# Performance work log

Hardware: AMD Instinct MI355X
Metric: run time of the kernel (lower is better)

Reference implementation:

```python
import jax, jax.numpy as jnp
import numpy as np

N = 100000      # nodes (accounts)
E = 500000      # edges (transactions)
F_NODE = 128
F_EDGE = 32
HEADS = 4
C = 64          # hidden_channels per head
HC = HEADS * C  # 256
OUT = 32
BN_EPS = 1e-5
NEG_SLOPE = 0.2


def setup_inputs() -> dict:
    key = jax.random.key(0)
    ks = jax.random.split(key, 24)
    rn = lambda k, shape, s=0.05: (jax.random.normal(k, shape, jnp.float32) * s)
    inp = {
        "x": jax.random.normal(ks[0], (N, F_NODE), jnp.float32),
        "edge_index": jax.random.randint(ks[1], (2, E), 0, N, dtype=jnp.int32),
        "edge_attr": jax.random.normal(ks[2], (E, F_EDGE), jnp.float32),
        # node_proj
        "Wp": rn(ks[3], (F_NODE, C)), "bp": jnp.zeros((C,), jnp.float32),
    }
    in_dims = [C, HC, HC]
    i = 4
    for l, d in enumerate(in_dims):
        inp[f"Wg{l}"] = rn(ks[i], (d, HC)); i += 1
        inp[f"as{l}"] = rn(ks[i], (HEADS, C)); i += 1
        inp[f"ad{l}"] = rn(ks[i], (HEADS, C)); i += 1
        inp[f"bg{l}"] = jnp.zeros((HC,), jnp.float32)
        inp[f"g{l}"] = jnp.ones((HC,), jnp.float32)   # BN gamma
        inp[f"be{l}"] = jnp.zeros((HC,), jnp.float32)  # BN beta
    inp["W1"] = rn(ks[i], (2 * HC + F_EDGE, OUT)); inp["b1"] = jnp.zeros((OUT,), jnp.float32)
    inp["W2"] = rn(ks[i + 1], (OUT, 1)); inp["b2"] = jnp.zeros((1,), jnp.float32)
    return inp


def _gat_layer(h, src, dst, Wg, att_s, att_d, bg):
    # PyG GATConv (concat=True, add_self_loops=False), eval mode (no dropout).
    xh = (h @ Wg).reshape(N, HEADS, C)                      # [N,H,C]
    a_s = jnp.sum(xh * att_s, axis=-1)                      # [N,H]
    a_d = jnp.sum(xh * att_d, axis=-1)                      # [N,H]
    e = jax.nn.leaky_relu(a_s[src] + a_d[dst], NEG_SLOPE)   # [E,H]
    m = jax.lax.stop_gradient(jax.ops.segment_max(e, dst, num_segments=N))
    ex = jnp.exp(e - m[dst])
    den = jax.ops.segment_sum(ex, dst, num_segments=N)      # [N,H]
    alpha = ex / (den[dst] + 1e-16)                         # softmax over in-edges of dst
    agg = jax.ops.segment_sum(xh[src] * alpha[:, :, None], dst, num_segments=N)
    return agg.reshape(N, HC) + bg


def _forward(x, edge_index, edge_attr, Wp, bp,
             Wg0, as0, ad0, bg0, g0, be0,
             Wg1, as1, ad1, bg1, g1, be1,
             Wg2, as2, ad2, bg2, g2, be2,
             W1, b1, W2, b2):
    src, dst = edge_index[0], edge_index[1]
    h = jax.nn.relu(x @ Wp + bp)                            # [N,64]
    bn_scale = 1.0 / jnp.sqrt(jnp.float32(1.0) + BN_EPS)    # BN eval: mean=0, var=1
    layers = [(Wg0, as0, ad0, bg0, g0, be0),
              (Wg1, as1, ad1, bg1, g1, be1),
              (Wg2, as2, ad2, bg2, g2, be2)]
    for Wg, a_s, a_d, bg, g, be in layers:
        hn = _gat_layer(h, src, dst, Wg, a_s, a_d, bg)
        hn = jax.nn.relu(hn * (g * bn_scale) + be)          # BatchNorm(eval) + ReLU
        h = h + hn if h.shape == hn.shape else hn           # residual (skipped at layer 0)
    # decode_edges: MLP(src_emb || dst_emb || edge_attr) without materializing the concat:
    W1s, W1d, W1e = W1[:HC], W1[HC:2 * HC], W1[2 * HC:]
    z = jax.nn.relu((h @ W1s)[src] + (h @ W1d)[dst] + edge_attr @ W1e + b1)  # [E,32]
    return (z @ W2 + b2)[:, 0]                              # [E] fraud logits


def reference(x, edge_index, edge_attr, Wp, bp,
              Wg0, as0, ad0, bg0, g0, be0,
              Wg1, as1, ad1, bg1, g1, be1,
              Wg2, as2, ad2, bg2, g2, be2,
              W1, b1, W2, b2):
    return _forward(x, edge_index, edge_attr, Wp, bp,
                    Wg0, as0, ad0, bg0, g0, be0,
                    Wg1, as1, ad1, bg1, g1, be1,
                    Wg2, as2, ad2, bg2, g2, be2,
                    W1, b1, W2, b2)
```

## Files before the change

kernel.cpp:

```cpp
#include <hip/hip_runtime.h>
#include <hip/hip_fp16.h>

#define NN 100000
#define EE 500000
#define F_NODE 128
#define F_EDGE 32
#define HEADS 4
#define CC 64
#define HC 256
#define OUTD 32
#define NEG_SLOPE 0.2f
#define BN_SCALE 0.9999950000374997f
#define NB_SCAN 391
#define MPAD 100096

using half8 = __attribute__((ext_vector_type(8))) _Float16;
using f32x4 = __attribute__((ext_vector_type(4))) float;

typedef const __attribute__((address_space(1))) void* gas_ptr;
typedef __attribute__((address_space(3))) void* las_ptr;

template<int K, int NOUT, int MODE, int ATT, int AF32>
__global__ __launch_bounds__(256, 2) void mgemm2(const __half* __restrict__ A,
                                                 const __half* __restrict__ Wt,
                                                 const float* __restrict__ bias,
                                                 __half* __restrict__ C,
                                                 const float* __restrict__ as_,
                                                 const float* __restrict__ ad_,
                                                 float* __restrict__ a_s,
                                                 float* __restrict__ a_d,
                                                 const float* __restrict__ A32) {
    constexpr int BM = 128;
    constexpr int BN = (NOUT >= 128) ? 128 : 64;
    constexpr int MI = 4;
    constexpr int NI = BN / 32;
    constexpr int KS = K / 64;
    constexpr int ABYTES = BM * 128;
    constexpr int BBYTES = BN * 128;
    __shared__ char smem[2 * (ABYTES + BBYTES)];

    const int tid  = threadIdx.x;
    const int wave = tid >> 6, lane = tid & 63;
    const int wr = wave >> 1, wc = wave & 1;
    const int lrow = lane & 15, kq = lane >> 4;
    const int m0 = blockIdx.x * BM;
    const int n0 = blockIdx.y * BN;
    const int srow = tid >> 3;
    const int sunit = tid & 7;
    const int wofs = (tid & 192) * 16;

    auto stageA16 = [&](int buf, int ks) {
        char* base = smem + buf * (ABYTES + BBYTES);
        const int kk = ks * 64;
#pragma unroll
        for (int it = 0; it < 4; ++it) {
            const int r = srow + it * 32;
            const __half* src = A + (size_t)(m0 + r) * K + kk + ((sunit ^ (r & 7)) << 3);
            __builtin_amdgcn_global_load_lds((gas_ptr)src,
                (las_ptr)(base + it * 4096 + wofs), 16, 0, 0);
        }
    };
    auto stageB = [&](int buf, int ks) {
        char* base = smem + buf * (ABYTES + BBYTES);
        const int kk = ks * 64;
#pragma unroll
        for (int it = 0; it < BN / 32; ++it) {
            const int r = srow + it * 32;
            const __half* src = Wt + (size_t)(n0 + r) * K + kk + ((sunit ^ (r & 7)) << 3);
            __builtin_amdgcn_global_load_lds((gas_ptr)src,
                (las_ptr)(base + ABYTES + it * 4096 + wofs), 16, 0, 0);
        }
    };

    float4 ar[4][2];
    auto loadA32 = [&](int ks) {
        const int kk = ks * 64;
#pragma unroll
        for (int it = 0; it < 4; ++it) {
            int rg = m0 + srow + it * 32;
            rg = (rg < NN) ? rg : NN - 1;
            const float* sp = A32 + (size_t)rg * K + kk + sunit * 8;
            ar[it][0] = *(const float4*)sp;
            ar[it][1] = *(const float4*)(sp + 4);
        }
    };
    auto writeA32 = [&](int buf) {
        char* base = smem + buf * (ABYTES + BBYTES);
#pragma unroll
        for (int it = 0; it < 4; ++it) {
            const int r = srow + it * 32;
            half8 hv;
            hv[0] = (_Float16)ar[it][0].x; hv[1] = (_Float16)ar[it][0].y;
            hv[2] = (_Float16)ar[it][0].z; hv[3] = (_Float16)ar[it][0].w;
            hv[4] = (_Float16)ar[it][1].x; hv[5] = (_Float16)ar[it][1].y;
            hv[6] = (_Float16)ar[it][1].z; hv[7] = (_Float16)ar[it][1].w;
            *(half8*)(base + r * 128 + ((sunit ^ (r & 7)) << 4)) = hv;
        }
    };

    f32x4 acc[MI][NI] = {};

    auto compute = [&](int buf) {
        const char* Ab = smem + buf * (ABYTES + BBYTES);
        const char* Bb = Ab + ABYTES;
#pragma unroll
        for (int k32 = 0; k32 < 2; ++k32) {
            const int ku = k32 * 4 + kq;
            half8 af[MI], bf[NI];
#pragma unroll
            for (int mi = 0; mi < MI; ++mi) {
                const int rr = wr * 64 + mi * 16 + lrow;
                af[mi] = *(const half8*)(Ab + rr * 128 + ((ku ^ (rr & 7)) << 4));
            }
#pragma unroll
            for (int ni = 0; ni < NI; ++ni) {
                const int rc = wc * (BN / 2) + ni * 16 + lrow;
                bf[ni] = *(const half8*)(Bb + rc * 128 + ((ku ^ (rc & 7)) << 4));
            }
#pragma unroll
            for (int mi = 0; mi < MI; ++mi)
#pragma unroll
                for (int ni = 0; ni < NI; ++ni)
                    acc[mi][ni] = __builtin_amdgcn_mfma_f32_16x16x32_f16(
                        af[mi], bf[ni], acc[mi][ni], 0, 0, 0);
        }
    };

    if constexpr (AF32) { loadA32(0); stageB(0, 0); writeA32(0); }
    else                { stageA16(0, 0); stageB(0, 0); }
    __syncthreads();
    int cur = 0;
#pragma unroll
    for (int ks = 0; ks < KS; ++ks) {
        if (ks + 1 < KS) {
            if constexpr (AF32) { loadA32(ks + 1); stageB(cur ^ 1, ks + 1); }
            else                { stageA16(cur ^ 1, ks + 1); stageB(cur ^ 1, ks + 1); }
        }
        compute(cur);
        if constexpr (AF32) { if (ks + 1 < KS) writeA32(cur ^ 1); }
        __syncthreads();
        cur ^= 1;
    }

    const int crow = kq * 4;
#pragma unroll
    for (int mi = 0; mi < MI; ++mi) {
#pragma unroll
        for (int ni = 0; ni < NI; ++ni) {
            const int col = n0 + wc * (BN / 2) + ni * 16 + lrow;
            float bcol = (MODE == 1) ? bias[col] : 0.f;
#pragma unroll
            for (int r = 0; r < 4; ++r) {
                float v = acc[mi][ni][r];
                if constexpr (MODE == 1) v = fmaxf(v + bcol, 0.f);
                const int row = m0 + wr * 64 + mi * 16 + crow + r;
                C[(size_t)row * NOUT + col] = __float2half(v);
            }
        }
    }

    if constexpr (ATT) {
        const int head = (n0 + wc * 64) >> 6;
        float wsv[NI], wdv[NI];
#pragma unroll
        for (int ni = 0; ni < NI; ++ni) {
            const int col = n0 + wc * (BN / 2) + ni * 16 + lrow;
            wsv[ni] = as_[col];
            wdv[ni] = ad_[col];
        }
#pragma unroll
        for (int mi = 0; mi < MI; ++mi) {
#pragma unroll
            for (int r = 0; r < 4; ++r) {
                float ss = 0.f, dd = 0.f;
#pragma unroll
                for (int ni = 0; ni < NI; ++ni) {
                    ss += acc[mi][ni][r] * wsv[ni];
                    dd += acc[mi][ni][r] * wdv[ni];
                }
#pragma unroll
                for (int off = 8; off >= 1; off >>= 1) {
                    ss += __shfl_xor(ss, off, 64);
                    dd += __shfl_xor(dd, off, 64);
                }
                if (lrow == 0) {
                    const int row = m0 + wr * 64 + mi * 16 + crow + r;
                    a_s[row * HEADS + head] = ss;
                    a_d[row * HEADS + head] = dd;
                }
            }
        }
    }
}

#define PREP_TOTAL (8192 + 16384 + 65536 + 65536 + 16384 + 1024)
__global__ __launch_bounds__(256) void prep_all(const float* __restrict__ Wp,
                                                const float* __restrict__ Wg0,
                                                const float* __restrict__ Wg1,
                                                const float* __restrict__ Wg2,
                                                const float* __restrict__ W1,
                                                __half* __restrict__ wpt,
                                                __half* __restrict__ wg0t,
                                                __half* __restrict__ wg1t,
                                                __half* __restrict__ wg2t,
                                                __half* __restrict__ w1t,
                                                __half* __restrict__ w1et) {
    int idx = blockIdx.x * 256 + threadIdx.x;
    if (idx < 8192) {
        int n = idx >> 7, k = idx & 127;
        wpt[idx] = __float2half(Wp[k * 64 + n]);
    } else if (idx < 24576) {
        int i = idx - 8192;
        int n = i >> 6, k = i & 63;
        wg0t[i] = __float2half(Wg0[k * 256 + n]);
    } else if (idx < 90112) {
        int i = idx - 24576;
        int n = i >> 8, k = i & 255;
        wg1t[i] = __float2half(Wg1[k * 256 + n]);
    } else if (idx < 155648) {
        int i = idx - 90112;
        int n = i >> 8, k = i & 255;
        wg2t[i] = __float2half(Wg2[k * 256 + n]);
    } else if (idx < 172032) {
        int i = idx - 155648;
        int n = i >> 8, k = i & 255;
        float v = (n < 32) ? W1[k * 32 + n] : W1[(256 + k) * 32 + (n - 32)];
        w1t[i] = __float2half(v);
    } else if (idx < PREP_TOTAL) {
        int i = idx - 172032;
        int n = i >> 5, k = i & 31;
        w1et[i] = __float2half(W1[2 * HC * OUTD + k * 32 + n]);
    }
}

__global__ __launch_bounds__(256) void csr_count(const int* __restrict__ dst,
                                                 int* __restrict__ deg,
                                                 int* __restrict__ pos) {
    int e = blockIdx.x * 256 + threadIdx.x;
    if (e >= EE) return;
    pos[e] = atomicAdd(deg + dst[e], 1);
}

__device__ __forceinline__ int wave_incl_scan(int v, int lane) {
#pragma unroll
    for (int off = 1; off < 64; off <<= 1) {
        int t = __shfl_up(v, off, 64);
        if (lane >= off) v += t;
    }
    return v;
}

__global__ __launch_bounds__(256) void scan1(const int* __restrict__ deg,
                                             int* __restrict__ rowptr,
                                             int* __restrict__ bsum) {
    int tid = threadIdx.x, n = blockIdx.x * 256 + tid;
    int lane = tid & 63, wave = tid >> 6;
    int d = (n < NN) ? deg[n] : 0;
    int v = wave_incl_scan(d, lane);
    __shared__ int ws[4];
    if (lane == 63) ws[wave] = v;
    __syncthreads();
    int woff = 0;
    for (int w = 0; w < wave; ++w) woff += ws[w];
    int incl = v + woff;
    if (n < NN) rowptr[n] = incl - d;
    if (tid == 255) bsum[blockIdx.x] = incl;
}

__global__ __launch_bounds__(512) void scan2(const int* __restrict__ bsum,
                                             int* __restrict__ boff) {
    int t = threadIdx.x;
    int lane = t & 63, wave = t >> 6;
    int d = (t < NB_SCAN) ? bsum[t] : 0;
    int v = wave_incl_scan(d, lane);
    __shared__ int ws[8];
    if (lane == 63) ws[wave] = v;
    __syncthreads();
    int woff = 0;
    for (int w = 0; w < wave; ++w) woff += ws[w];
    if (t < NB_SCAN) boff[t] = v + woff - d;
}

__global__ __launch_bounds__(256) void scan3(int* __restrict__ rowptr,
                                             const int* __restrict__ boff) {
    int n = blockIdx.x * 256 + threadIdx.x;
    if (n == 0) rowptr[NN] = EE;
    if (n < NN) rowptr[n] += boff[blockIdx.x];
}

__global__ __launch_bounds__(256) void csr_scatter(const int* __restrict__ src,
                                                   const int* __restrict__ dst,
                                                   const int* __restrict__ rowptr,
                                                   const int* __restrict__ pos,
                                                   int* __restrict__ srcs) {
    int e = blockIdx.x * 256 + threadIdx.x;
    if (e >= EE) return;
    srcs[rowptr[dst[e]] + pos[e]] = src[e];
}

__global__ __launch_bounds__(256) void gather_agg(const int* __restrict__ rowptr,
                                                  const int* __restrict__ srcs,
                                                  const float* __restrict__ a_s,
                                                  const float* __restrict__ a_d,
                                                  const __half* __restrict__ xh,
                                                  const float* __restrict__ bg,
                                                  const float* __restrict__ g,
                                                  const float* __restrict__ be,
                                                  __half* __restrict__ h,
                                                  int residual) {
    const int n = blockIdx.x * 4 + (threadIdx.x >> 6);
    const int lane = threadIdx.x & 63;
    const int hl = lane >> 5;
    const int l5 = lane & 31;
    const int hd = l5 >> 3;
    const int c0 = l5 * 8;

    const int start = rowptr[n], end = rowptr[n + 1];
    const float adv = a_d[n * HEADS + hd];

    float acc[8] = {};
    float den = 0.f;

    for (int i = start + hl; i < end; i += 8) {
        int  j1 = (i + 2 < end) ? i + 2 : i;
        int  j2 = (i + 4 < end) ? i + 4 : i;
        int  j3 = (i + 6 < end) ? i + 6 : i;
        const int s0 = srcs[i], s1 = srcs[j1], s2 = srcs[j2], s3 = srcs[j3];

        float v0 = a_s[s0 * HEADS + hd] + adv;
        float v1 = a_s[s1 * HEADS + hd] + adv;
        float v2 = a_s[s2 * HEADS + hd] + adv;
        float v3 = a_s[s3 * HEADS + hd] + adv;
        v0 = fmaxf(v0, v0 * NEG_SLOPE);
        v1 = fmaxf(v1, v1 * NEG_SLOPE);
        v2 = fmaxf(v2, v2 * NEG_SLOPE);
        v3 = fmaxf(v3, v3 * NEG_SLOPE);
        float e0 = __expf(v0);
        float e1 = (i + 2 < end) ? __expf(v1) : 0.f;
        float e2 = (i + 4 < end) ? __expf(v2) : 0.f;
        float e3 = (i + 6 < end) ? __expf(v3) : 0.f;

        half8 r0 = *(const half8*)(xh + (size_t)s0 * HC + c0);
        half8 r1 = *(const half8*)(xh + (size_t)s1 * HC + c0);
        half8 r2 = *(const half8*)(xh + (size_t)s2 * HC + c0);
        half8 r3 = *(const half8*)(xh + (size_t)s3 * HC + c0);

#pragma unroll
        for (int k = 0; k < 8; ++k)
            acc[k] += e0 * (float)r0[k] + e1 * (float)r1[k]
                    + e2 * (float)r2[k] + e3 * (float)r3[k];
        den += e0 + e1 + e2 + e3;
    }

    den += __shfl_xor(den, 32, 64);
#pragma unroll
    for (int k = 0; k < 8; ++k) acc[k] += __shfl_xor(acc[k], 32, 64);

    if (hl != 0) return;
    const float inv = 1.f / (den + 1e-16f);

    float bgv[8], gv[8], bev[8];
    *(float4*)(bgv)     = *(const float4*)(bg + c0);
    *(float4*)(bgv + 4) = *(const float4*)(bg + c0 + 4);
    *(float4*)(gv)      = *(const float4*)(g + c0);
    *(float4*)(gv + 4)  = *(const float4*)(g + c0 + 4);
    *(float4*)(bev)     = *(const float4*)(be + c0);
    *(float4*)(bev + 4) = *(const float4*)(be + c0 + 4);

    half8* hp = (half8*)(h + (size_t)n * HC + c0);
    float r[8];
#pragma unroll
    for (int k = 0; k < 8; ++k)
        r[k] = fmaxf((acc[k] * inv + bgv[k]) * (gv[k] * BN_SCALE) + bev[k], 0.f);
    if (residual) {
        half8 old = *hp;
#pragma unroll
        for (int k = 0; k < 8; ++k) r[k] += (float)old[k];
    }
    half8 o;
#pragma unroll
    for (int k = 0; k < 8; ++k) o[k] = (_Float16)r[k];
    __builtin_nontemporal_store(o, hp);
}

__global__ __launch_bounds__(256) void edge_final(const float* __restrict__ ea,
                                                  const __half* __restrict__ w1et,
                                                  const float* __restrict__ b1,
                                                  const int* __restrict__ src,
                                                  const int* __restrict__ dst,
                                                  const __half* __restrict__ hshd,
                                                  const float* __restrict__ W2,
                                                  const float* __restrict__ b2,
                                                  float* __restrict__ out) {
    __shared__ float zl[64][36];
    const int wave = threadIdx.x >> 6, lane = threadIdx.x & 63;
    const int e0 = blockIdx.x * 64;
    const int lrow = lane & 15, kofs = (lane >> 4) * 8;

    int er = e0 + wave * 16 + lrow;
    if (er >= EE) er = EE - 1;
    const float* ap = ea + (size_t)er * F_EDGE + kofs;
    float4 f0 = *(const float4*)ap;
    float4 f1 = *(const float4*)(ap + 4);
    half8 a;
    a[0] = (_Float16)f0.x; a[1] = (_Float16)f0.y;
    a[2] = (_Float16)f0.z; a[3] = (_Float16)f0.w;
    a[4] = (_Float16)f1.x; a[5] = (_Float16)f1.y;
    a[6] = (_Float16)f1.z; a[7] = (_Float16)f1.w;

    half8 b0 = *(const half8*)(w1et + (size_t)lrow * 32 + kofs);
    half8 b1v = *(const half8*)(w1et + (size_t)(16 + lrow) * 32 + kofs);
    f32x4 acc0 = {}, acc1 = {};
    acc0 = __builtin_amdgcn_mfma_f32_16x16x32_f16(a, b0,  acc0, 0, 0, 0);
    acc1 = __builtin_amdgcn_mfma_f32_16x16x32_f16(a, b1v, acc1, 0, 0, 0);

    const int crow = (lane >> 4) * 4;
    const float bc0 = b1[lrow], bc1 = b1[16 + lrow];
#pragma unroll
    for (int r = 0; r < 4; ++r) {
        zl[wave * 16 + crow + r][lrow]      = acc0[r] + bc0;
        zl[wave * 16 + crow + r][16 + lrow] = acc1[r] + bc1;
    }
    __syncthreads();

    const int el = threadIdx.x >> 2, j0 = (threadIdx.x & 3) * 8;
    const int e = e0 + el;
    const bool ok = e < EE;
    const int s = ok ? src[e] : 0;
    const int d = ok ? dst[e] : 0;

    half8 hs = *(const half8*)(hshd + (size_t)s * 64 + j0);
    half8 hdv = *(const half8*)(hshd + (size_t)d * 64 + 32 + j0);
    float w2v[8];
    *(float4*)(w2v)     = *(const float4*)(W2 + j0);
    *(float4*)(w2v + 4) = *(const float4*)(W2 + j0 + 4);
    float4 z0 = *(const float4*)&zl[el][j0];
    float4 z1 = *(const float4*)&zl[el][j0 + 4];

    float acc = 0.f;
    const float* zp0 = &z0.x;
    const float* zp1 = &z1.x;
#pragma unroll
    for (int i = 0; i < 4; ++i) {
        float z = zp0[i] + (float)hs[i] + (float)hdv[i];
        acc += fmaxf(z, 0.f) * w2v[i];
    }
#pragma unroll
    for (int i = 0; i < 4; ++i) {
        float z = zp1[i] + (float)hs[4 + i] + (float)hdv[4 + i];
        acc += fmaxf(z, 0.f) * w2v[4 + i];
    }
    acc += __shfl_xor(acc, 1, 64);
    acc += __shfl_xor(acc, 2, 64);
    if (ok && (threadIdx.x & 3) == 0) out[e] = acc + b2[0];
}

extern "C" void kernel_launch(void* const* d_in, const int* in_sizes, int n_in,
                              void* d_out, int out_size, void* d_ws, size_t ws_size,
                              hipStream_t stream) {
    const float* x  = (const float*)d_in[0];
    const int*   ei = (const int*)d_in[1];
    const float* ea = (const float*)d_in[2];
    const float* Wp = (const float*)d_in[3];
    const float* bp = (const float*)d_in[4];
    const float* W1 = (const float*)d_in[23];
    const float* b1 = (const float*)d_in[24];
    const float* W2 = (const float*)d_in[25];
    const float* b2 = (const float*)d_in[26];
    const int* src = ei;
    const int* dst = ei + EE;

    float* ws = (float*)d_ws;
    __half* h      = (__half*)(ws);
    __half* xh     = (__half*)(ws + 12820000);
    __half* h0     = (__half*)(ws + 32050000);
    __half* hshd   = (__half*)(ws + 35260000);
    float*  a_s    = ws + 38470000;
    float*  a_d    = ws + 38880000;
    int*    rowptr = (int*)(ws + 41270000);
    int*    deg    = (int*)(ws + 41380000);
    int*    pos    = (int*)(ws + 41480000);
    int*    srcs   = (int*)(ws + 42490000);
    int*    bsum   = (int*)(ws + 42990000);
    int*    boff   = (int*)(ws + 42991000);
    __half* wpt    = (__half*)(ws + 42992000);
    __half* wg0t   = (__half*)(ws + 43000000);
    __half* wg1t   = (__half*)(ws + 43010000);
    __half* wg2t   = (__half*)(ws + 43045000);
    __half* w1t    = (__half*)(ws + 43080000);
    __half* w1et   = (__half*)(ws + 43090000);
    float*  out    = (float*)d_out;

    const int MB = MPAD / 128;

    hipMemsetAsync(deg, 0, (size_t)NN * sizeof(int), stream);
    prep_all<<<(PREP_TOTAL + 255) / 256, 256, 0, stream>>>(
        Wp, (const float*)d_in[5], (const float*)d_in[11], (const float*)d_in[17],
        W1, wpt, wg0t, wg1t, wg2t, w1t, w1et);
    csr_count<<<(EE + 255) / 256, 256, 0, stream>>>(dst, deg, pos);
    scan1<<<NB_SCAN, 256, 0, stream>>>(deg, rowptr, bsum);
    scan2<<<1, 512, 0, stream>>>(bsum, boff);
    scan3<<<NB_SCAN, 256, 0, stream>>>(rowptr, boff);
    csr_scatter<<<(EE + 255) / 256, 256, 0, stream>>>(src, dst, rowptr, pos, srcs);

    mgemm2<F_NODE, 64, 1, 0, 1><<<dim3(MB, 1), 256, 0, stream>>>(
        nullptr, wpt, bp, h0, nullptr, nullptr, nullptr, nullptr, x);

    const __half* wgt_l[3] = {wg0t, wg1t, wg2t};
    for (int l = 0; l < 3; ++l) {
        const float* as_ = (const float*)d_in[6 + 6 * l];
        const float* ad_ = (const float*)d_in[7 + 6 * l];
        const float* bg  = (const float*)d_in[8 + 6 * l];
        const float* g   = (const float*)d_in[9 + 6 * l];
        const float* be  = (const float*)d_in[10 + 6 * l];

        if (l == 0) {
            mgemm2<CC, HC, 0, 1, 0><<<dim3(MB, 2), 256, 0, stream>>>(
                h0, wgt_l[0], nullptr, xh, as_, ad_, a_s, a_d, nullptr);
        } else {
            mgemm2<HC, HC, 0, 1, 0><<<dim3(MB, 2), 256, 0, stream>>>(
                h, wgt_l[l], nullptr, xh, as_, ad_, a_s, a_d, nullptr);
        }

        gather_agg<<<NN / 4, 256, 0, stream>>>(rowptr, srcs, a_s, a_d, xh,
                                               bg, g, be, h, l > 0 ? 1 : 0);
    }

    mgemm2<HC, 64, 0, 0, 0><<<dim3(MB, 1), 256, 0, stream>>>(
        h, w1t, nullptr, hshd, nullptr, nullptr, nullptr, nullptr, nullptr);

    edge_final<<<(EE + 63) / 64, 256, 0, stream>>>(ea, w1et, b1, src, dst,
                                                   hshd, W2, b2, out);
}
```

Measured before the change: 374.3 us.

## Reorder layer-0 GAT to aggregate 64-dim inputs before projecting with block-diagonal weights

Layer 0 now computes attention logits directly from the 64-dim projected features using precomputed Wg0·att vectors. It aggregates the 64-wide h0 rows per head instead of the 256-wide xh rows, then applies a block-diagonal 256x256 GEMM whose epilogue adds bias, BatchNorm and ReLU. The aim is to cut gather bandwidth in the first layer by a factor of four. The cost is two extra small kernels and a GEMM that is four times larger than before, three quarters of it multiplying zeros. Rounding changes slightly because the aggregated values are stored as fp16 before projection.

```diff
diff --git a/kernel.cpp b/kernel.cpp
--- a/kernel.cpp
+++ b/kernel.cpp
@@ -29,7 +29,10 @@
                                                  const float* __restrict__ ad_,
                                                  float* __restrict__ a_s,
                                                  float* __restrict__ a_d,
-                                                 const float* __restrict__ A32) {
+                                                 const float* __restrict__ A32,
+                                                 const float* __restrict__ bg,
+                                                 const float* __restrict__ g,
+                                                 const float* __restrict__ be) {
     constexpr int BM = 128;
     constexpr int BN = (NOUT >= 128) ? 128 : 64;
     constexpr int MI = 4;
@@ -149,10 +152,15 @@
         for (int ni = 0; ni < NI; ++ni) {
             const int col = n0 + wc * (BN / 2) + ni * 16 + lrow;
             float bcol = (MODE == 1) ? bias[col] : 0.f;
+            float bnb = 0.f, bng = 0.f, bne = 0.f;
+            if constexpr (MODE == 2) {
+                bnb = bg[col]; bng = g[col] * BN_SCALE; bne = be[col];
+            }
 #pragma unroll
             for (int r = 0; r < 4; ++r) {
                 float v = acc[mi][ni][r];
                 if constexpr (MODE == 1) v = fmaxf(v + bcol, 0.f);
+                if constexpr (MODE == 2) v = fmaxf((v + bnb) * bng + bne, 0.f);
                 const int row = m0 + wr * 64 + mi * 16 + crow + r;
                 C[(size_t)row * NOUT + col] = __float2half(v);
             }
@@ -193,43 +201,89 @@
     }
 }
 
-#define PREP_TOTAL (8192 + 16384 + 65536 + 65536 + 16384 + 1024)
+#define PREP_TOTAL (8192 + 65536 + 65536 + 65536 + 16384 + 1024 + 256 + 256)
 __global__ __launch_bounds__(256) void prep_all(const float* __restrict__ Wp,
                                                 const float* __restrict__ Wg0,
                                                 const float* __restrict__ Wg1,
                                                 const float* __restrict__ Wg2,
                                                 const float* __restrict__ W1,
+                                                const float* __restrict__ as0,
+                                                const float* __restrict__ ad0,
                                                 __half* __restrict__ wpt,
-                                                __half* __restrict__ wg0t,
+                                                __half* __restrict__ w0bdt,
                                                 __half* __restrict__ wg1t,
                                                 __half* __restrict__ wg2t,
                                                 __half* __restrict__ w1t,
-                                                __half* __restrict__ w1et) {
+                                                __half* __restrict__ w1et,
+                                                float* __restrict__ asf,
+                                                float* __restrict__ adf) {
     int idx = blockIdx.x * 256 + threadIdx.x;
     if (idx < 8192) {
         int n = idx >> 7, k = idx & 127;
         wpt[idx] = __float2half(Wp[k * 64 + n]);
-    } else if (idx < 24576) {
+    } else if (idx < 73728) {
         int i = idx - 8192;
-        int n = i >> 6, k = i & 63;
-        wg0t[i] = __float2half(Wg0[k * 256 + n]);
-    } else if (idx < 90112) {
-        int i = idx - 24576;
+        int n = i >> 8, k = i & 255;
+        float v = ((n >> 6) == (k >> 6)) ? Wg0[(k & 63) * 256 + n] : 0.f;
+        w0bdt[i] = __float2half(v);
+    } else if (idx < 139264) {
+        int i = idx - 73728;
         int n = i >> 8, k = i & 255;
         wg1t[i] = __float2half(Wg1[k * 256 + n]);
-    } else if (idx < 155648) {
-        int i = idx - 90112;
+    } else if (idx < 204800) {
+        int i = idx - 139264;
         int n = i >> 8, k = i & 255;
         wg2t[i] = __float2half(Wg2[k * 256 + n]);
-    } else if (idx < 172032) {
-        int i = idx - 155648;
+    } else if (idx < 221184) {
+        int i = idx - 204800;
         int n = i >> 8, k = i & 255;
         float v = (n < 32) ? W1[k * 32 + n] : W1[(256 + k) * 32 + (n - 32)];
         w1t[i] = __float2half(v);
-    } else if (idx < PREP_TOTAL) {
-        int i = idx - 172032;
+    } else if (idx < 222208) {
+        int i = idx - 221184;
         int n = i >> 5, k = i & 31;
         w1et[i] = __float2half(W1[2 * HC * OUTD + k * 32 + n]);
+    } else if (idx < 222464) {
+        int i = idx - 222208;
+        int k = i >> 2, hh = i & 3;
+        float s = 0.f;
+        for (int c = 0; c < 64; ++c)
+            s += Wg0[k * 256 + hh * 64 + c] * as0[hh * 64 + c];
+        asf[i] = s;
+    } else if (idx < PREP_TOTAL) {
+        int i = idx - 222464;
+        int k = i >> 2, hh = i & 3;
+        float s = 0.f;
+        for (int c = 0; c < 64; ++c)
+            s += Wg0[k * 256 + hh * 64 + c] * ad0[hh * 64 + c];
+        adf[i] = s;
+    }
+}
+
+__global__ __launch_bounds__(256) void att0(const __half* __restrict__ h0,
+                                            const float* __restrict__ asf,
+                                            const float* __restrict__ adf,
+                                            float* __restrict__ a_s,
+                                            float* __restrict__ a_d) {
+    const int n = blockIdx.x * 4 + (threadIdx.x >> 6);
+    const int lane = threadIdx.x & 63;
+    const float v = __half2float(h0[(size_t)n * 64 + lane]);
+    float4 af = *(const float4*)(asf + lane * 4);
+    float4 df = *(const float4*)(adf + lane * 4);
+    float p0 = v * af.x, p1 = v * af.y, p2 = v * af.z, p3 = v * af.w;
+    float q0 = v * df.x, q1 = v * df.y, q2 = v * df.z, q3 = v * df.w;
+#pragma unroll
+    for (int m = 32; m >= 1; m >>= 1) {
+        p0 += __shfl_xor(p0, m, 64); p1 += __shfl_xor(p1, m, 64);
+        p2 += __shfl_xor(p2, m, 64); p3 += __shfl_xor(p3, m, 64);
+        q0 += __shfl_xor(q0, m, 64); q1 += __shfl_xor(q1, m, 64);
+        q2 += __shfl_xor(q2, m, 64); q3 += __shfl_xor(q3, m, 64);
+    }
+    if (lane == 0) {
+        a_s[n * 4 + 0] = p0; a_s[n * 4 + 1] = p1;
+        a_s[n * 4 + 2] = p2; a_s[n * 4 + 3] = p3;
+        a_d[n * 4 + 0] = q0; a_d[n * 4 + 1] = q1;
+        a_d[n * 4 + 2] = q2; a_d[n * 4 + 3] = q3;
     }
 }
 
@@ -296,6 +350,67 @@
     int e = blockIdx.x * 256 + threadIdx.x;
     if (e >= EE) return;
     srcs[rowptr[dst[e]] + pos[e]] = src[e];
+}
+
+__global__ __launch_bounds__(256) void gather_l0(const int* __restrict__ rowptr,
+                                                 const int* __restrict__ srcs,
+                                                 const float* __restrict__ a_s,
+                                                 const float* __restrict__ a_d,
+                                                 const __half* __restrict__ h0,
+                                                 __half* __restrict__ acc16) {
+    const int n = blockIdx.x * 4 + (threadIdx.x >> 6);
+    const int lane = threadIdx.x & 63;
+    const int hl = lane >> 5;
+    const int l5 = lane & 31;
+    const int hd = l5 >> 3;
+    const int k0 = (l5 & 7) * 8;
+    const int start = rowptr[n], end = rowptr[n + 1];
+    const float adv = a_d[n * HEADS + hd];
+
+    float acc[8] = {};
+    float den = 0.f;
+
+    for (int i = start + hl; i < end; i += 8) {
+        int  j1 = (i + 2 < end) ? i + 2 : i;
+        int  j2 = (i + 4 < end) ? i + 4 : i;
+        int  j3 = (i + 6 < end) ? i + 6 : i;
+        const int s0 = srcs[i], s1 = srcs[j1], s2 = srcs[j2], s3 = srcs[j3];
+
+        float v0 = a_s[s0 * HEADS + hd] + adv;
+        float v1 = a_s[s1 * HEADS + hd] + adv;
+        float v2 = a_s[s2 * HEADS + hd] + adv;
+        float v3 = a_s[s3 * HEADS + hd] + adv;
+        v0 = fmaxf(v0, v0 * NEG_SLOPE);
+        v1 = fmaxf(v1, v1 * NEG_SLOPE);
+        v2 = fmaxf(v2, v2 * NEG_SLOPE);
+        v3 = fmaxf(v3, v3 * NEG_SLOPE);
+        float e0 = __expf(v0);
+        float e1 = (i + 2 < end) ? __expf(v1) : 0.f;
+        float e2 = (i + 4 < end) ? __expf(v2) : 0.f;
+        float e3 = (i + 6 < end) ? __expf(v3) : 0.f;
+
+        half8 r0 = *(const half8*)(h0 + (size_t)s0 * 64 + k0);
+        half8 r1 = *(const half8*)(h0 + (size_t)s1 * 64 + k0);
+        half8 r2 = *(const half8*)(h0 + (size_t)s2 * 64 + k0);
+        half8 r3 = *(const half8*)(h0 + (size_t)s3 * 64 + k0);
+
+#pragma unroll
+        for (int k = 0; k < 8; ++k)
+            acc[k] += e0 * (float)r0[k] + e1 * (float)r1[k]
+                    + e2 * (float)r2[k] + e3 * (float)r3[k];
+        den += e0 + e1 + e2 + e3;
+    }
+
+    den += __shfl_xor(den, 32, 64);
+#pragma unroll
+    for (int k = 0; k < 8; ++k) acc[k] += __shfl_xor(acc[k], 32, 64);
+
+    if (hl != 0) return;
+    const float inv = 1.f / (den + 1e-16f);
+    half8 o;
+#pragma unroll
+    for (int k = 0; k < 8; ++k) o[k] = (_Float16)(acc[k] * inv);
+    *(half8*)(acc16 + (size_t)n * HC + l5 * 8) = o;
 }
 
 __global__ __launch_bounds__(256) void gather_agg(const int* __restrict__ rowptr,
@@ -484,11 +599,13 @@
     int*    bsum   = (int*)(ws + 42990000);
     int*    boff   = (int*)(ws + 42991000);
     __half* wpt    = (__half*)(ws + 42992000);
-    __half* wg0t   = (__half*)(ws + 43000000);
-    __half* wg1t   = (__half*)(ws + 43010000);
-    __half* wg2t   = (__half*)(ws + 43045000);
-    __half* w1t    = (__half*)(ws + 43080000);
-    __half* w1et   = (__half*)(ws + 43090000);
+    __half* w0bdt  = (__half*)(ws + 43000000);
+    __half* wg1t   = (__half*)(ws + 43035000);
+    __half* wg2t   = (__half*)(ws + 43070000);
+    __half* w1t    = (__half*)(ws + 43105000);
+    __half* w1et   = (__half*)(ws + 43115000);
+    float*  asf    = ws + 43120000;
+    float*  adf    = ws + 43121000;
     float*  out    = (float*)d_out;
 
     const int MB = MPAD / 128;
@@ -496,7 +613,8 @@
     hipMemsetAsync(deg, 0, (size_t)NN * sizeof(int), stream);
     prep_all<<<(PREP_TOTAL + 255) / 256, 256, 0, stream>>>(
         Wp, (const float*)d_in[5], (const float*)d_in[11], (const float*)d_in[17],
-        W1, wpt, wg0t, wg1t, wg2t, w1t, w1et);
+        W1, (const float*)d_in[6], (const float*)d_in[7],
+        wpt, w0bdt, wg1t, wg2t, w1t, w1et, asf, adf);
     csr_count<<<(EE + 255) / 256, 256, 0, stream>>>(dst, deg, pos);
     scan1<<<NB_SCAN, 256, 0, stream>>>(deg, rowptr, bsum);
     scan2<<<1, 512, 0, stream>>>(bsum, boff);
@@ -504,30 +622,33 @@
     csr_scatter<<<(EE + 255) / 256, 256, 0, stream>>>(src, dst, rowptr, pos, srcs);
 
     mgemm2<F_NODE, 64, 1, 0, 1><<<dim3(MB, 1), 256, 0, stream>>>(
-        nullptr, wpt, bp, h0, nullptr, nullptr, nullptr, nullptr, x);
-
-    const __half* wgt_l[3] = {wg0t, wg1t, wg2t};
-    for (int l = 0; l < 3; ++l) {
+        nullptr, wpt, bp, h0, nullptr, nullptr, nullptr, nullptr, x,
+        nullptr, nullptr, nullptr);
+
+    att0<<<NN / 4, 256, 0, stream>>>(h0, asf, adf, a_s, a_d);
+    gather_l0<<<NN / 4, 256, 0, stream>>>(rowptr, srcs, a_s, a_d, h0, xh);
+    mgemm2<HC, HC, 2, 0, 0><<<dim3(MB, 2), 256, 0, stream>>>(
+        xh, w0bdt, nullptr, h, nullptr, nullptr, nullptr, nullptr, nullptr,
+        (const float*)d_in[8], (const float*)d_in[9], (const float*)d_in[10]);
+
+    const __half* wgt_l[2] = {wg1t, wg2t};
+    for (int l = 1; l < 3; ++l) {
         const float* as_ = (const float*)d_in[6 + 6 * l];
         const float* ad_ = (const float*)d_in[7 + 6 * l];
         const float* bg  = (const float*)d_in[8 + 6 * l];
         const float* g   = (const float*)d_in[9 + 6 * l];
         const float* be  = (const float*)d_in[10 + 6 * l];
 
-        if (l == 0) {
-            mgemm2<CC, HC, 0, 1, 0><<<dim3(MB, 2), 256, 0, stream>>>(
-                h0, wgt_l[0], nullptr, xh, as_, ad_, a_s, a_d, nullptr);
-        } else {
-            mgemm2<HC, HC, 0, 1, 0><<<dim3(MB, 2), 256, 0, stream>>>(
-                h, wgt_l[l], nullptr, xh, as_, ad_, a_s, a_d, nullptr);
-        }
-
+        mgemm2<HC, HC, 0, 1, 0><<<dim3(MB, 2), 256, 0, stream>>>(
+            h, wgt_l[l - 1], nullptr, xh, as_, ad_, a_s, a_d, nullptr,
+            nullptr, nullptr, nullptr);
         gather_agg<<<NN / 4, 256, 0, stream>>>(rowptr, srcs, a_s, a_d, xh,
-                                               bg, g, be, h, l > 0 ? 1 : 0);
+                                               bg, g, be, h, 1);
     }
 
     mgemm2<HC, 64, 0, 0, 0><<<dim3(MB, 1), 256, 0, stream>>>(
-        h, w1t, nullptr, hshd, nullptr, nullptr, nullptr, nullptr, nullptr);
+        h, w1t, nullptr, hshd, nullptr, nullptr, nullptr, nullptr, nullptr,
+        nullptr, nullptr, nullptr);
 
     edge_final<<<(EE + 63) / 64, 256, 0, stream>>>(ea, w1et, b1, src, dst,
                                                    hshd, W2, b2, out);
```

After: 417.8 us. 11.6% more time.
